# Kernel optimization log

Measured on AMD Instinct MI355X. Metric: run time of the kernel, lower is better.

Reference implementation:

```python
import jax, jax.numpy as jnp
import numpy as np

TAU = 0.5      # init kwarg tau
LAMBD = 0.5    # init kwarg lambd
N, D, C = 4096, 1024, 512


def setup_inputs() -> dict:
    key = jax.random.key(0)
    k1, k2, k3 = jax.random.split(key, 3)
    return {
        "layer_embeds": jax.random.normal(k1, (N, D), dtype=jnp.float32),
        "y_true": jax.random.randint(k2, (N,), 0, C),
        "y_pred": jax.random.normal(k3, (N, C), dtype=jnp.float32),
    }


def _clce(x, y_true, y_pred):
    n = x.shape[0]
    # pairwise cosine similarity via one matmul (torch eps = 1e-8)
    norms = jnp.clip(jnp.linalg.norm(x, axis=1, keepdims=True), 1e-8)
    xn = x / norms
    sim = (xn @ xn.T + 1.0) * 0.5 * TAU          # [N, N]

    same = y_true[:, None] == y_true[None, :]    # diagonal is always True
    eye = jnp.eye(n, dtype=bool)
    pos_mask = same & ~eye                        # candidate positives (j != i)
    neg_mask = ~same                              # negatives (excludes diagonal)

    # slot 0: similarity to the FIRST positive j (in j order), else stays 0
    first_pos = jnp.argmax(pos_mask, axis=1)
    has_pos = pos_mask.any(axis=1)
    slot0 = jnp.where(has_pos,
                      jnp.take_along_axis(sim, first_pos[:, None], axis=1)[:, 0],
                      0.0)

    # negatives packed left-to-right into columns 1..; unfilled slots stay 0
    cum = jnp.cumsum(neg_mask, axis=1)            # 1-based slot per negative
    cols = jnp.where(neg_mask, cum, 2 * n - 1)    # non-negatives -> sink col
    rows = jnp.arange(n)[:, None]
    loss_temp = jnp.zeros((n, 2 * n), dtype=sim.dtype)
    loss_temp = loss_temp.at[rows, cols].add(jnp.where(neg_mask, sim, 0.0))
    loss_temp = loss_temp.at[:, 0].set(slot0)
    loss_temp = loss_temp[:, : 2 * n - 1]         # drop sink column -> [N, 2N-1]

    cl = -jax.nn.log_softmax(loss_temp, axis=1)[:, 0]
    cl = cl.sum() / n

    logp = jax.nn.log_softmax(y_pred, axis=1)
    ce = -jnp.take_along_axis(logp, y_true[:, None], axis=1).mean()

    return LAMBD * cl + (1.0 - LAMBD) * ce


def reference(layer_embeds, y_true, y_pred):
    return _clce(layer_embeds, y_true, y_pred)
```

## Files before the change

kernel.cpp:

```cpp
#include <hip/hip_runtime.h>
#include <hip/hip_bf16.h>

#define NR 4096
#define DIM 1024
#define NCLS 512

typedef __attribute__((ext_vector_type(4))) float f32x4;
typedef __attribute__((ext_vector_type(8))) int v8i;

static __device__ __forceinline__ unsigned int q4(float v) {
  unsigned int s = (v < 0.f) ? 8u : 0u;
  float a = fabsf(v);
  unsigned int c;
  if (a < 0.25f) c = 0;
  else if (a < 0.75f) c = 1;
  else if (a < 1.25f) c = 2;
  else if (a < 1.75f) c = 3;
  else if (a < 2.5f) c = 4;
  else if (a < 3.5f) c = 5;
  else if (a < 5.0f) c = 6;
  else c = 7;
  return s | c;
}

__global__ __launch_bounds__(256) void k_prep(const float* __restrict__ x,
                                              const int* __restrict__ y,
                                              const float* __restrict__ yp,
                                              unsigned char* __restrict__ xnp,
                                              int* __restrict__ cnt,
                                              int* __restrict__ fpos,
                                              float* __restrict__ slot0,
                                              float* __restrict__ ce,
                                              float* __restrict__ out) {
  const int b = blockIdx.x;
  const int tid = threadIdx.x;
  if (b < 1024) {
    int row = b * 4 + (tid >> 6);
    int lane = tid & 63;
    const float4* xr = reinterpret_cast<const float4*>(x + (size_t)row * DIM);
    float4 v[4];
    float s = 0.f;
#pragma unroll
    for (int it = 0; it < 4; ++it) {
      v[it] = xr[it * 64 + lane];
      s += v[it].x * v[it].x + v[it].y * v[it].y + v[it].z * v[it].z + v[it].w * v[it].w;
    }
#pragma unroll
    for (int d = 1; d < 64; d <<= 1) s += __shfl_xor(s, d);
    float inv = 32.0f / fmaxf(sqrtf(s), 1e-8f);
    unsigned char* xo = xnp + (size_t)row * 512;
#pragma unroll
    for (int it = 0; it < 4; ++it) {
      int k0 = (it * 64 + lane) * 4;
      int pos = (k0 >> 7) * 64 + ((k0 >> 5) & 3) * 16 + ((k0 & 31) >> 1);
      unsigned int n0 = q4(v[it].x * inv), n1 = q4(v[it].y * inv),
                   n2 = q4(v[it].z * inv), n3 = q4(v[it].w * inv);
      unsigned short pk =
          (unsigned short)(n0 | (n1 << 4) | (n2 << 8) | (n3 << 12));
      *(unsigned short*)(xo + pos) = pk;
    }
  } else if (b < 2048) {
    int row = (b - 1024) * 4 + (tid >> 6);
    int lane = tid & 63;
    const float4* p = reinterpret_cast<const float4*>(yp + (size_t)row * NCLS);
    float4 v0 = p[lane], v1 = p[lane + 64];
    float m = fmaxf(fmaxf(fmaxf(v0.x, v0.y), fmaxf(v0.z, v0.w)),
                    fmaxf(fmaxf(v1.x, v1.y), fmaxf(v1.z, v1.w)));
#pragma unroll
    for (int d = 1; d < 64; d <<= 1) m = fmaxf(m, __shfl_xor(m, d));
    float s = __expf(v0.x - m) + __expf(v0.y - m) + __expf(v0.z - m) + __expf(v0.w - m) +
              __expf(v1.x - m) + __expf(v1.y - m) + __expf(v1.z - m) + __expf(v1.w - m);
#pragma unroll
    for (int d = 1; d < 64; d <<= 1) s += __shfl_xor(s, d);
    if (lane == 0) {
      float py = yp[(size_t)row * NCLS + y[row]];
      ce[row] = logf(s) + m - py;
    }
  } else {
    __shared__ int ys[NR];
    __shared__ int scnt[NCLS], sm1[NCLS], sm2[NCLS];
    for (int j = tid; j < NR; j += 256) ys[j] = y[j];
    for (int c = tid; c < NCLS; c += 256) { scnt[c] = 0; sm1[c] = NR; sm2[c] = NR; }
    __syncthreads();
    for (int i = tid; i < NR; i += 256) {
      int c = ys[i];
      atomicAdd(&scnt[c], 1);
      atomicMin(&sm1[c], i);
    }
    __syncthreads();
    for (int i = tid; i < NR; i += 256) {
      int c = ys[i];
      if (sm1[c] != i) atomicMin(&sm2[c], i);
    }
    __syncthreads();
    for (int i = tid; i < NR; i += 256) {
      int c = ys[i];
      int m1 = sm1[c];
      int j = (m1 == i) ? ((sm2[c] >= NR) ? -1 : sm2[c]) : m1;
      fpos[i] = j;
      slot0[i] = 0.f;
    }
    for (int c = tid; c < NCLS; c += 256) cnt[c] = scnt[c];
    if (tid == 0) out[0] = 0.f;
  }
}


#define STAGE(SSLOT, GROWBASE, KT)                                               \
  {                                                                              \
    const char* _src = (const char*)xnp +                                        \
        (size_t)((GROWBASE) + srow) * 512 + (size_t)(KT) * 64 + scol;            \
    __builtin_amdgcn_global_load_lds(                                            \
        (const __attribute__((address_space(1))) void*)_src,                     \
        (__attribute__((address_space(3))) void*)(lds + (SSLOT) + tid * 16),     \
        16, 0, 0);                                                               \
  }

#define PHASE(BUFB, RP, LOADB, SSLOT, SBASE, SKT, VM)                            \
  {                                                                              \
    _Pragma("unroll") for (int mm = 0; mm < 2; ++mm) {                           \
      int4 t4 = *(const int4*)(lds + (BUFB) + ABaseW +                           \
                               ((RP) * 2 + mm) * 1024);                          \
      v8i tv = {t4.x, t4.y, t4.z, t4.w, 0, 0, 0, 0};                             \
      afr[mm] = tv;                                                              \
    }                                                                            \
    if (LOADB) {                                                                 \
      _Pragma("unroll") for (int nf = 0; nf < 2; ++nf) {                         \
        int4 t4 = *(const int4*)(lds + (BUFB) + BBaseW + nf * 1024);             \
        v8i tv = {t4.x, t4.y, t4.z, t4.w, 0, 0, 0, 0};                           \
        bfr[nf] = tv;                                                            \
      }                                                                          \
    }                                                                            \
    STAGE(SSLOT, SBASE, SKT)                                                     \
    if (VM) asm volatile("s_waitcnt vmcnt(1)" ::: "memory");                     \
    __builtin_amdgcn_s_barrier();                                                \
    asm volatile("s_waitcnt lgkmcnt(0)" ::: "memory");                           \
    __builtin_amdgcn_sched_barrier(0);                                           \
    __builtin_amdgcn_s_setprio(1);                                               \
    _Pragma("unroll") for (int mm = 0; mm < 2; ++mm)                             \
      _Pragma("unroll") for (int nf = 0; nf < 2; ++nf)                           \
        acc[(RP) * 2 + mm][nf] = __builtin_amdgcn_mfma_scale_f32_16x16x128_f8f6f4( \
            afr[mm], bfr[nf], acc[(RP) * 2 + mm][nf], 4, 4,                      \
            0, 0x7F7F7F7F, 0, 0x7F7F7F7F);                                       \
    __builtin_amdgcn_s_setprio(0);                                               \
    __builtin_amdgcn_sched_barrier(0);                                           \
    __builtin_amdgcn_s_barrier();                                                \
  }

__global__ __launch_bounds__(512, 2) void k_gemm(const unsigned char* __restrict__ xnp,
                                                 const int* __restrict__ y,
                                                 const int* __restrict__ fpos,
                                                 float* __restrict__ part,
                                                 float* __restrict__ slot0) {
  __shared__ char lds[32768];
  const int tid = threadIdx.x;
  const int w = tid >> 6, lane = tid & 63;
  const int wr = w >> 2, wcn = w & 3;
  const int r0 = lane & 15, klo = lane >> 4;

  const int bid = blockIdx.x;
  int t = (bid & 7) * 66 + (bid >> 3), rb = 0;
  while (t >= 32 - rb) { t -= 32 - rb; ++rb; }
  const int cb = rb + t;
  const int rowbase = rb * 128, colbase = cb * 128;
  const bool offd = (rb != cb);

  const int kread = (klo * 16) ^ ((r0 & 3) << 4);
  const int ABaseW = wr * 4096 + r0 * 64 + kread;
  const int BBaseW = 8192 + wcn * 2048 + r0 * 64 + kread;

  int srow, scol;
  {
    int D = tid * 16;
    int L = D ^ (((D >> 6) & 3) << 4);
    srow = L >> 6;
    scol = L & 63;
  }

  f32x4 acc[4][2] = {};

  STAGE(8192, colbase, 0)
  STAGE(0, rowbase, 0)
  STAGE(24576, colbase, 1)
  asm volatile("s_waitcnt vmcnt(1)" ::: "memory");
  __builtin_amdgcn_s_barrier();

  for (int i = 0; i < 4; ++i) {
    const int t1 = 2 * i + 1;
    const int tn = (2 * i + 2 < 8) ? 2 * i + 2 : 7;
    const int tn1 = (2 * i + 3 < 8) ? 2 * i + 3 : 7;
    v8i afr[2], bfr[2];
    PHASE(0,     0, 1, 16384, rowbase, t1, 0)
    PHASE(0,     1, 0, 8192,  colbase, tn, 1)
    PHASE(16384, 0, 1, 0,     rowbase, tn, 0)
    PHASE(16384, 1, 0, 24576, colbase, tn1, 1)
  }

  asm volatile("s_waitcnt vmcnt(0)" ::: "memory");
  __syncthreads();

  int* yrow_s = (int*)lds;
  int* ycol_s = (int*)(lds + 512);
  int* frow_s = (int*)(lds + 1024);
  int* fcol_s = (int*)(lds + 1536);
  float* rsum = (float*)(lds + 2048);
  float* csum = (float*)(lds + 4096);
  if (tid < 128) {
    yrow_s[tid] = y[rowbase + tid];
    frow_s[tid] = fpos[rowbase + tid];
  } else if (tid < 256) {
    ycol_s[tid - 128] = y[colbase + tid - 128];
    fcol_s[tid - 128] = fpos[colbase + tid - 128];
  }
  __syncthreads();

  float csn[2] = {0.f, 0.f};
#pragma unroll
  for (int m = 0; m < 4; ++m) {
    float rs[4] = {0.f, 0.f, 0.f, 0.f};
    int rloc[4], yr[4], fr[4];
#pragma unroll
    for (int reg = 0; reg < 4; ++reg) {
      rloc[reg] = wr * 64 + m * 16 + klo * 4 + reg;
      yr[reg] = yrow_s[rloc[reg]];
      fr[reg] = frow_s[rloc[reg]];
    }
#pragma unroll
    for (int nf = 0; nf < 2; ++nf) {
      int cl = wcn * 32 + nf * 16 + r0;
      int yc = ycol_s[cl];
      int fc = fcol_s[cl];
      int gc = colbase + cl;
#pragma unroll
      for (int reg = 0; reg < 4; ++reg) {
        float sv = acc[m][nf][reg] * (1.0f / 4096.f) + 0.25f;
        float e = (yr[reg] == yc) ? 0.f : __expf(sv);
        rs[reg] += e;
        csn[nf] += e;
        int gr = rowbase + rloc[reg];
        if (fr[reg] == gc) slot0[gr] = sv;
        if (offd && fc == gr) slot0[gc] = sv;
      }
    }
#pragma unroll
    for (int d = 1; d < 16; d <<= 1)
#pragma unroll
      for (int reg = 0; reg < 4; ++reg) rs[reg] += __shfl_xor(rs[reg], d);
    if (r0 == 0) {
#pragma unroll
      for (int reg = 0; reg < 4; ++reg)
        rsum[rloc[reg] * 4 + wcn] = rs[reg];
    }
  }
#pragma unroll
  for (int nf = 0; nf < 2; ++nf) {
    csn[nf] += __shfl_xor(csn[nf], 16);
    csn[nf] += __shfl_xor(csn[nf], 32);
  }
  if (klo == 0) {
#pragma unroll
    for (int nf = 0; nf < 2; ++nf)
      csum[(wcn * 32 + nf * 16 + r0) * 2 + wr] = csn[nf];
  }
  __syncthreads();
  if (tid < 128) {
    part[(size_t)cb * NR + rowbase + tid] =
        rsum[tid * 4] + rsum[tid * 4 + 1] + rsum[tid * 4 + 2] + rsum[tid * 4 + 3];
    if (offd)
      part[(size_t)rb * NR + colbase + tid] = csum[tid * 2] + csum[tid * 2 + 1];
  }
}

__global__ __launch_bounds__(256) void k_final(const float* __restrict__ part,
                                               const float* __restrict__ slot0,
                                               const int* __restrict__ cnt,
                                               const int* __restrict__ y,
                                               const float* __restrict__ ce,
                                               float* __restrict__ out) {
  __shared__ float red[256];
  const int tid = threadIdx.x;
  const int r = blockIdx.x * 256 + tid;
  float S = 0.f;
#pragma unroll
  for (int b = 0; b < 32; ++b) S += part[(size_t)b * NR + r];
  float s0 = slot0[r];
  float zeros = 4094.0f + (float)cnt[y[r]];
  float cl = logf(__expf(s0) + S + zeros) - s0;
  red[tid] = 0.5f * (cl + ce[r]);
  __syncthreads();
  for (int s = 128; s > 0; s >>= 1) {
    if (tid < s) red[tid] += red[tid + s];
    __syncthreads();
  }
  if (tid == 0) atomicAdd(out, red[0] / (float)NR);
}

extern "C" void kernel_launch(void* const* d_in, const int* in_sizes, int n_in,
                              void* d_out, int out_size, void* d_ws, size_t ws_size,
                              hipStream_t stream) {
  const float* x = (const float*)d_in[0];
  const int* y = (const int*)d_in[1];
  const float* yp = (const float*)d_in[2];
  float* out = (float*)d_out;

  char* w = (char*)d_ws;
  unsigned char* xnp = (unsigned char*)w;
  int* cnt = (int*)(w + 2097152);
  int* fpos = (int*)(w + 2099200);
  float* slot0 = (float*)(w + 2115584);
  float* part = (float*)(w + 2131968);
  float* ce = (float*)(w + 2656256);

  k_prep<<<2049, 256, 0, stream>>>(x, y, yp, xnp, cnt, fpos, slot0, ce, out);
  k_gemm<<<528, 512, 0, stream>>>(xnp, y, fpos, part, slot0);
  k_final<<<16, 256, 0, stream>>>(part, slot0, cnt, y, ce, out);
}
```

Measured before the change: 45.21 us.

## Replace ping-pong LDS pipeline with four-slot ring buffer and deeper prefetch

```diff
diff --git a/kernel.cpp b/kernel.cpp
--- a/kernel.cpp
+++ b/kernel.cpp
@@ -106,45 +106,22 @@
 }
 
 
-#define STAGE(SSLOT, GROWBASE, KT)                                               \
+#define STAGE2(SLOT, KT)                                                         \
   {                                                                              \
-    const char* _src = (const char*)xnp +                                        \
-        (size_t)((GROWBASE) + srow) * 512 + (size_t)(KT) * 64 + scol;            \
+    const char* _sa = (const char*)xnp +                                         \
+        (size_t)(rowbase + srow) * 512 + (size_t)(KT) * 64 + scol;               \
     __builtin_amdgcn_global_load_lds(                                            \
-        (const __attribute__((address_space(1))) void*)_src,                     \
-        (__attribute__((address_space(3))) void*)(lds + (SSLOT) + tid * 16),     \
+        (const __attribute__((address_space(1))) void*)_sa,                      \
+        (__attribute__((address_space(3))) void*)(lds + (SLOT) * 16384 +         \
+                                                  tid * 16),                     \
         16, 0, 0);                                                               \
-  }
-
-#define PHASE(BUFB, RP, LOADB, SSLOT, SBASE, SKT, VM)                            \
-  {                                                                              \
-    _Pragma("unroll") for (int mm = 0; mm < 2; ++mm) {                           \
-      int4 t4 = *(const int4*)(lds + (BUFB) + ABaseW +                           \
-                               ((RP) * 2 + mm) * 1024);                          \
-      v8i tv = {t4.x, t4.y, t4.z, t4.w, 0, 0, 0, 0};                             \
-      afr[mm] = tv;                                                              \
-    }                                                                            \
-    if (LOADB) {                                                                 \
-      _Pragma("unroll") for (int nf = 0; nf < 2; ++nf) {                         \
-        int4 t4 = *(const int4*)(lds + (BUFB) + BBaseW + nf * 1024);             \
-        v8i tv = {t4.x, t4.y, t4.z, t4.w, 0, 0, 0, 0};                           \
-        bfr[nf] = tv;                                                            \
-      }                                                                          \
-    }                                                                            \
-    STAGE(SSLOT, SBASE, SKT)                                                     \
-    if (VM) asm volatile("s_waitcnt vmcnt(1)" ::: "memory");                     \
-    __builtin_amdgcn_s_barrier();                                                \
-    asm volatile("s_waitcnt lgkmcnt(0)" ::: "memory");                           \
-    __builtin_amdgcn_sched_barrier(0);                                           \
-    __builtin_amdgcn_s_setprio(1);                                               \
-    _Pragma("unroll") for (int mm = 0; mm < 2; ++mm)                             \
-      _Pragma("unroll") for (int nf = 0; nf < 2; ++nf)                           \
-        acc[(RP) * 2 + mm][nf] = __builtin_amdgcn_mfma_scale_f32_16x16x128_f8f6f4( \
-            afr[mm], bfr[nf], acc[(RP) * 2 + mm][nf], 4, 4,                      \
-            0, 0x7F7F7F7F, 0, 0x7F7F7F7F);                                       \
-    __builtin_amdgcn_s_setprio(0);                                               \
-    __builtin_amdgcn_sched_barrier(0);                                           \
-    __builtin_amdgcn_s_barrier();                                                \
+    const char* _sb = (const char*)xnp +                                         \
+        (size_t)(colbase + srow) * 512 + (size_t)(KT) * 64 + scol;               \
+    __builtin_amdgcn_global_load_lds(                                            \
+        (const __attribute__((address_space(1))) void*)_sb,                      \
+        (__attribute__((address_space(3))) void*)(lds + (SLOT) * 16384 + 8192 +  \
+                                                  tid * 16),                     \
+        16, 0, 0);                                                               \
   }
 
 __global__ __launch_bounds__(512, 2) void k_gemm(const unsigned char* __restrict__ xnp,
@@ -152,16 +129,16 @@
                                                  const int* __restrict__ fpos,
                                                  float* __restrict__ part,
                                                  float* __restrict__ slot0) {
-  __shared__ char lds[32768];
+  __shared__ char lds[65536];
   const int tid = threadIdx.x;
   const int w = tid >> 6, lane = tid & 63;
   const int wr = w >> 2, wcn = w & 3;
   const int r0 = lane & 15, klo = lane >> 4;
 
   const int bid = blockIdx.x;
-  int t = (bid & 7) * 66 + (bid >> 3), rb = 0;
-  while (t >= 32 - rb) { t -= 32 - rb; ++rb; }
-  const int cb = rb + t;
+  int t0 = (bid & 7) * 66 + (bid >> 3), rb = 0;
+  while (t0 >= 32 - rb) { t0 -= 32 - rb; ++rb; }
+  const int cb = rb + t0;
   const int rowbase = rb * 128, colbase = cb * 128;
   const bool offd = (rb != cb);
 
@@ -179,21 +156,41 @@
 
   f32x4 acc[4][2] = {};
 
-  STAGE(8192, colbase, 0)
-  STAGE(0, rowbase, 0)
-  STAGE(24576, colbase, 1)
-  asm volatile("s_waitcnt vmcnt(1)" ::: "memory");
-  __builtin_amdgcn_s_barrier();
-
-  for (int i = 0; i < 4; ++i) {
-    const int t1 = 2 * i + 1;
-    const int tn = (2 * i + 2 < 8) ? 2 * i + 2 : 7;
-    const int tn1 = (2 * i + 3 < 8) ? 2 * i + 3 : 7;
-    v8i afr[2], bfr[2];
-    PHASE(0,     0, 1, 16384, rowbase, t1, 0)
-    PHASE(0,     1, 0, 8192,  colbase, tn, 1)
-    PHASE(16384, 0, 1, 0,     rowbase, tn, 0)
-    PHASE(16384, 1, 0, 24576, colbase, tn1, 1)
+  STAGE2(0, 0)
+  STAGE2(1, 1)
+  STAGE2(2, 2)
+
+#pragma unroll
+  for (int t = 0; t < 8; ++t) {
+    asm volatile("s_waitcnt vmcnt(4)" ::: "memory");
+    __builtin_amdgcn_s_barrier();
+    {
+      const int kt = (t + 3 < 8) ? t + 3 : 7;
+      STAGE2((t + 3) & 3, kt)
+    }
+    const int bufb = (t & 3) * 16384;
+    v8i afr[4], bfr[2];
+#pragma unroll
+    for (int mm = 0; mm < 4; ++mm) {
+      int4 t4 = *(const int4*)(lds + bufb + ABaseW + mm * 1024);
+      v8i tv = {t4.x, t4.y, t4.z, t4.w, 0, 0, 0, 0};
+      afr[mm] = tv;
+    }
+#pragma unroll
+    for (int nf = 0; nf < 2; ++nf) {
+      int4 t4 = *(const int4*)(lds + bufb + BBaseW + nf * 1024);
+      v8i tv = {t4.x, t4.y, t4.z, t4.w, 0, 0, 0, 0};
+      bfr[nf] = tv;
+    }
+    __builtin_amdgcn_s_setprio(1);
+#pragma unroll
+    for (int mm = 0; mm < 4; ++mm)
+#pragma unroll
+      for (int nf = 0; nf < 2; ++nf)
+        acc[mm][nf] = __builtin_amdgcn_mfma_scale_f32_16x16x128_f8f6f4(
+            afr[mm], bfr[nf], acc[mm][nf], 4, 4,
+            0, 0x7F7F7F7F, 0, 0x7F7F7F7F);
+    __builtin_amdgcn_s_setprio(0);
   }
 
   asm volatile("s_waitcnt vmcnt(0)" ::: "memory");
```

After: 45.45 us. About the same (+0.5%).
